# Kernel tuning notes

Measured on AMD Instinct MI355X. Metric: run time of the kernel, lower is better.

The kernel has to match this reference:

```python
import jax, jax.numpy as jnp
import numpy as np


def setup_inputs() -> dict:
    key = jax.random.key(0)
    k1, k2 = jax.random.split(key)
    n_nodes, d_feat, n_edges = 100000, 48, 1600000
    x = jax.random.normal(k1, (n_nodes, d_feat), dtype=jnp.float32)
    edge_index = jax.random.randint(k2, (2, n_edges), 0, n_nodes, dtype=jnp.int64)
    return {"x": x, "edge_index": edge_index, "batch_size": 65536}


def reference(x, edge_index, batch_size):
    # adj = SparseTensor.from_edge_index(edge_index): adj[row, col] = 1 with
    # row = edge_index[0] (src), col = edge_index[1] (dst).
    # adj.t() @ x  ->  out[i] = sum over edges (src -> i) of x[src]
    src, dst = edge_index[0], edge_index[1]
    n_nodes = x.shape[0]
    # memory-bound gather + scatter-add (SpMM, sum aggregation)
    x_neighbors_sum = jax.ops.segment_sum(x[src], dst, num_segments=n_nodes)
    node_labels = jnp.concatenate(
        (x[:batch_size, :], x_neighbors_sum[:batch_size, :]), axis=-1
    )
    return node_labels
```

## Files before the change

kernel.cpp:

```cpp
#include <hip/hip_runtime.h>

#define DFEAT 48
#define OUTW  96
#define NBINB 256
#define BINTH 512
#define SORTCAP 6272
#define NBUCK2 512
#define RBITS 7
#define NROWS 128
#define RAWCAP 2560
#define HCAP 1536


__global__ __launch_bounds__(BINTH)
void bin_k(const int* __restrict__ ei, int n_edges, int batch, int chunk,
           unsigned short* __restrict__ starts, unsigned int* __restrict__ regions) {
    __shared__ int cnt[NBUCK2];
    __shared__ int off[NBUCK2];
    __shared__ int cur[NBUCK2];
    __shared__ unsigned int sorted[SORTCAP];
    const int t = threadIdx.x;
    const int b = blockIdx.x;
    const int beg = b * chunk;
    const int end = min(beg + chunk, n_edges);

    cnt[t] = 0;
    __syncthreads();
    for (int e = beg + t; e < end; e += BINTH) {
        int dst = ei[n_edges + e];
        if (dst < batch) atomicAdd(&cnt[dst >> RBITS], 1);
    }
    __syncthreads();
    int v = cnt[t];
    off[t] = v;
    __syncthreads();
    for (int d = 1; d < NBUCK2; d <<= 1) {
        int tv = (t >= d) ? off[t - d] : 0;
        __syncthreads();
        off[t] += tv;
        __syncthreads();
    }
    int excl = off[t] - v;
    int tot  = off[NBUCK2 - 1];
    __syncthreads();
    off[t] = excl;
    cur[t] = excl;
    starts[t * NBINB + b] = (unsigned short)excl;
    if (t == 0) starts[NBUCK2 * NBINB + b] = (unsigned short)tot;
    __syncthreads();
    for (int e = beg + t; e < end; e += BINTH) {
        int dst = ei[n_edges + e];
        if (dst < batch) {
            int src = ei[e];
            int pos = atomicAdd(&cur[dst >> RBITS], 1);
            sorted[pos] = ((unsigned int)(dst & (NROWS - 1)) << 17) | (unsigned int)src;
        }
    }
    __syncthreads();
    unsigned int* reg = regions + (size_t)b * chunk;
    for (int i = t; i < tot; i += BINTH) reg[i] = sorted[i];
}

__global__ __launch_bounds__(512)
void reduce_k(const float* __restrict__ x,
              const unsigned short* __restrict__ starts,
              const unsigned int* __restrict__ regions,
              float* __restrict__ out, int batch, int chunk) {
    __shared__ unsigned int raw[RAWCAP];
    __shared__ int csr[HCAP];
    __shared__ int rs[NBINB], rp[NBINB], rl[NBINB];
    __shared__ int cnt[64], off[65], cur[64];
    __shared__ int Tsh;
    const int t = threadIdx.x;
    const int kb = blockIdx.x >> 1;
    const int half = blockIdx.x & 1;

    if (t < NBINB) {
        int s0 = starts[kb * NBINB + t];
        int s1 = starts[(kb + 1) * NBINB + t];
        rs[t] = s0;
        rl[t] = s1 - s0;
        rp[t] = s1 - s0;
    }
    __syncthreads();
    for (int d = 1; d < NBINB; d <<= 1) {
        int tv = (t < NBINB && t >= d) ? rp[t - d] : 0;
        __syncthreads();
        if (t < NBINB) rp[t] += tv;
        __syncthreads();
    }
    if (t == NBINB - 1) Tsh = rp[t];
    __syncthreads();
    const int T = min(Tsh, RAWCAP);
    if (t < NBINB) rp[t] -= rl[t];
    __syncthreads();
    {
        int r = t >> 1, h = t & 1;
        int len = rl[r], base = rp[r];
        const unsigned int* reg = regions + (size_t)r * chunk + rs[r];
        for (int i = h; i < len; i += 2) {
            int p = base + i;
            if (p < RAWCAP) raw[p] = reg[i];
        }
    }
    __syncthreads();
    if (t < 64) cnt[t] = 0;
    __syncthreads();
    for (int i = t; i < T; i += 512) {
        int rw = raw[i] >> 17;
        if ((rw >> 6) == half) atomicAdd(&cnt[rw & 63], 1);
    }
    __syncthreads();
    int v = (t < 64) ? cnt[t] : 0;
    if (t < 64) off[t] = v;
    __syncthreads();
    for (int d = 1; d < 64; d <<= 1) {
        int tv = (t < 64 && t >= d) ? off[t - d] : 0;
        __syncthreads();
        if (t < 64) off[t] += tv;
        __syncthreads();
    }
    if (t == 63) off[64] = off[63];
    int excl = (t < 64) ? off[t] - v : 0;
    __syncthreads();
    if (t < 64) { off[t] = excl; cur[t] = excl; }
    __syncthreads();
    for (int i = t; i < T; i += 512) {
        unsigned int p = raw[i];
        int rw = p >> 17;
        if ((rw >> 6) == half) {
            int pos = atomicAdd(&cur[rw & 63], 1);
            if (pos < HCAP) csr[pos] = (int)(p & 0x1FFFFu);
        }
    }
    __syncthreads();
    const int wave = t >> 6, lane = t & 63;
    if (lane < DFEAT) {
        for (int r = wave; r < 64; r += 8) {
            int row = kb * NROWS + half * 64 + r;
            if (row >= batch) break;
            int s0 = off[r], s1 = min(off[r + 1], HCAP);
            float acc = 0.f;
            int e = s0;
            for (; e + 4 <= s1; e += 4) {
                float v0 = x[(size_t)csr[e + 0] * DFEAT + lane];
                float v1 = x[(size_t)csr[e + 1] * DFEAT + lane];
                float v2 = x[(size_t)csr[e + 2] * DFEAT + lane];
                float v3 = x[(size_t)csr[e + 3] * DFEAT + lane];
                acc += v0 + v1 + v2 + v3;
            }
            for (; e < s1; ++e) acc += x[(size_t)csr[e] * DFEAT + lane];
            out[(size_t)row * OUTW + lane]         = x[(size_t)row * DFEAT + lane];
            out[(size_t)row * OUTW + DFEAT + lane] = acc;
        }
    }
}


#define D4   12
#define ROW4 24

__global__ void init_out_kernel(const float4* __restrict__ x4,
                                float4* __restrict__ out4, int batch) {
    int idx = blockIdx.x * blockDim.x + threadIdx.x;
    int total = batch * ROW4;
    if (idx >= total) return;
    int row = idx / ROW4;
    int c   = idx - row * ROW4;
    float4 v;
    if (c < D4) v = x4[row * D4 + c];
    else        v = make_float4(0.f, 0.f, 0.f, 0.f);
    out4[idx] = v;
}

__global__ void scatter_edges_kernel(const float4* __restrict__ x4,
                                     const int* __restrict__ ei,
                                     float* __restrict__ out,
                                     int n_edges, int batch) {
    int tid = blockIdx.x * blockDim.x + threadIdx.x;
    int e = tid / D4;
    int q = tid - e * D4;
    if (e >= n_edges) return;
    int dst = ei[n_edges + e];
    if (dst >= batch) return;
    int src = ei[e];
    float4 v = x4[src * D4 + q];
    float* p = out + (size_t)dst * OUTW + DFEAT + q * 4;
    atomicAdd(p + 0, v.x);
    atomicAdd(p + 1, v.y);
    atomicAdd(p + 2, v.z);
    atomicAdd(p + 3, v.w);
}


extern "C" void kernel_launch(void* const* d_in, const int* in_sizes, int n_in,
                              void* d_out, int out_size, void* d_ws, size_t ws_size,
                              hipStream_t stream) {
    const float* x  = (const float*)d_in[0];
    const int*   ei = (const int*)d_in[1];
    float* out = (float*)d_out;

    const int n_edges = in_sizes[1] / 2;
    const int batch   = out_size / OUTW;
    const int n_nodes = in_sizes[0] / DFEAT;
    const int chunk   = (n_edges + NBINB - 1) / NBINB;
    const int nbuck   = (batch + NROWS - 1) / NROWS;

    size_t starts_bytes = (size_t)(NBUCK2 + 1) * NBINB * sizeof(unsigned short);
    size_t need = starts_bytes + (size_t)NBINB * chunk * sizeof(unsigned int);

    bool ok = ws_size >= need && chunk <= SORTCAP && n_nodes <= (1 << 17) &&
              batch <= NBUCK2 * NROWS && nbuck >= 1;

    if (ok) {
        unsigned short* starts = (unsigned short*)d_ws;
        unsigned int* regions = (unsigned int*)((char*)d_ws + starts_bytes);
        bin_k<<<NBINB, BINTH, 0, stream>>>(ei, n_edges, batch, chunk, starts, regions);
        reduce_k<<<nbuck * 2, 512, 0, stream>>>(x, starts, regions, out, batch, chunk);
    } else {
        {
            int total = batch * ROW4;
            int grid = (total + 255) / 256;
            init_out_kernel<<<grid, 256, 0, stream>>>((const float4*)x,
                                                      (float4*)out, batch);
        }
        {
            long long total = (long long)n_edges * D4;
            long long grid = (total + 255) / 256;
            scatter_edges_kernel<<<(int)grid, 256, 0, stream>>>(
                (const float4*)x, ei, out, n_edges, batch);
        }
    }
}
```

Measured before the change: 135.6 us.

## Gather neighbors from fp16 copy of x, double binning blocks, register-cache edges

The binning kernel now also converts x to fp16 in workspace, and the reduce kernel gathers neighbour rows from that half-precision copy while still accumulating in fp32. The number of binning blocks doubles to 512 and each thread keeps its edges in registers, so edge_index is read once instead of twice. The reduce kernel's per-bin copy is reassigned to one thread per bin. This halves gather bytes but adds a full pass over x for conversion and introduces fp16 rounding error in the neighbour sums.

```diff
diff --git a/kernel.cpp b/kernel.cpp
--- a/kernel.cpp
+++ b/kernel.cpp
@@ -1,10 +1,12 @@
 #include <hip/hip_runtime.h>
+#include <hip/hip_fp16.h>
 
 #define DFEAT 48
 #define OUTW  96
-#define NBINB 256
+#define NBINB 512
 #define BINTH 512
-#define SORTCAP 6272
+#define EPT   7
+#define SORTCAP 3328
 #define NBUCK2 512
 #define RBITS 7
 #define NROWS 128
@@ -12,93 +14,119 @@
 #define HCAP 1536
 
 
+static __device__ __forceinline__ unsigned short f2h(float f) {
+    __half h = __float2half_rn(f);
+    return *reinterpret_cast<unsigned short*>(&h);
+}
+static __device__ __forceinline__ float h2f(unsigned short u) {
+    __half_raw hr; hr.x = u;
+    return __half2float(*reinterpret_cast<__half*>(&hr));
+}
+
 __global__ __launch_bounds__(BINTH)
 void bin_k(const int* __restrict__ ei, int n_edges, int batch, int chunk,
-           unsigned short* __restrict__ starts, unsigned int* __restrict__ regions) {
+           const float4* __restrict__ x4, int nx4, uint2* __restrict__ xh4,
+           unsigned short* __restrict__ starts, unsigned int* __restrict__ regions,
+           int use_half) {
     __shared__ int cnt[NBUCK2];
-    __shared__ int off[NBUCK2];
     __shared__ int cur[NBUCK2];
     __shared__ unsigned int sorted[SORTCAP];
     const int t = threadIdx.x;
     const int b = blockIdx.x;
+
+    if (use_half) {
+        for (int i = b * BINTH + t; i < nx4; i += NBINB * BINTH) {
+            float4 v = x4[i];
+            unsigned short h0 = f2h(v.x), h1 = f2h(v.y);
+            unsigned short h2 = f2h(v.z), h3 = f2h(v.w);
+            xh4[i] = make_uint2((unsigned)h0 | ((unsigned)h1 << 16),
+                                (unsigned)h2 | ((unsigned)h3 << 16));
+        }
+    }
+
     const int beg = b * chunk;
     const int end = min(beg + chunk, n_edges);
 
+    unsigned int pay[EPT];
+    int bkt[EPT];
+    #pragma unroll
+    for (int i = 0; i < EPT; i++) {
+        bkt[i] = -1;
+        int e = beg + t + i * BINTH;
+        if (e < end) {
+            int dst = ei[n_edges + e];
+            if (dst < batch) {
+                int src = ei[e];
+                bkt[i] = dst >> RBITS;
+                pay[i] = ((unsigned)(dst & (NROWS - 1)) << 17) | (unsigned)src;
+            }
+        }
+    }
     cnt[t] = 0;
     __syncthreads();
-    for (int e = beg + t; e < end; e += BINTH) {
-        int dst = ei[n_edges + e];
-        if (dst < batch) atomicAdd(&cnt[dst >> RBITS], 1);
-    }
+    #pragma unroll
+    for (int i = 0; i < EPT; i++)
+        if (bkt[i] >= 0) atomicAdd(&cnt[bkt[i]], 1);
     __syncthreads();
     int v = cnt[t];
-    off[t] = v;
+    cur[t] = v;
     __syncthreads();
     for (int d = 1; d < NBUCK2; d <<= 1) {
-        int tv = (t >= d) ? off[t - d] : 0;
-        __syncthreads();
-        off[t] += tv;
-        __syncthreads();
-    }
-    int excl = off[t] - v;
-    int tot  = off[NBUCK2 - 1];
-    __syncthreads();
-    off[t] = excl;
+        int tv = (t >= d) ? cur[t - d] : 0;
+        __syncthreads();
+        cur[t] += tv;
+        __syncthreads();
+    }
+    int tot  = cur[NBUCK2 - 1];
+    int excl = cur[t] - v;
+    __syncthreads();
     cur[t] = excl;
     starts[t * NBINB + b] = (unsigned short)excl;
     if (t == 0) starts[NBUCK2 * NBINB + b] = (unsigned short)tot;
     __syncthreads();
-    for (int e = beg + t; e < end; e += BINTH) {
-        int dst = ei[n_edges + e];
-        if (dst < batch) {
-            int src = ei[e];
-            int pos = atomicAdd(&cur[dst >> RBITS], 1);
-            sorted[pos] = ((unsigned int)(dst & (NROWS - 1)) << 17) | (unsigned int)src;
-        }
-    }
+    #pragma unroll
+    for (int i = 0; i < EPT; i++)
+        if (bkt[i] >= 0) {
+            int pos = atomicAdd(&cur[bkt[i]], 1);
+            sorted[pos] = pay[i];
+        }
     __syncthreads();
     unsigned int* reg = regions + (size_t)b * chunk;
     for (int i = t; i < tot; i += BINTH) reg[i] = sorted[i];
 }
 
 __global__ __launch_bounds__(512)
-void reduce_k(const float* __restrict__ x,
+void reduce_k(const float* __restrict__ x, const unsigned short* __restrict__ xh,
               const unsigned short* __restrict__ starts,
               const unsigned int* __restrict__ regions,
-              float* __restrict__ out, int batch, int chunk) {
+              float* __restrict__ out, int batch, int chunk, int use_half) {
     __shared__ unsigned int raw[RAWCAP];
     __shared__ int csr[HCAP];
     __shared__ int rs[NBINB], rp[NBINB], rl[NBINB];
     __shared__ int cnt[64], off[65], cur[64];
-    __shared__ int Tsh;
     const int t = threadIdx.x;
     const int kb = blockIdx.x >> 1;
     const int half = blockIdx.x & 1;
 
-    if (t < NBINB) {
+    {
         int s0 = starts[kb * NBINB + t];
         int s1 = starts[(kb + 1) * NBINB + t];
-        rs[t] = s0;
-        rl[t] = s1 - s0;
-        rp[t] = s1 - s0;
+        rs[t] = s0; rl[t] = s1 - s0; rp[t] = s1 - s0;
     }
     __syncthreads();
     for (int d = 1; d < NBINB; d <<= 1) {
-        int tv = (t < NBINB && t >= d) ? rp[t - d] : 0;
-        __syncthreads();
-        if (t < NBINB) rp[t] += tv;
-        __syncthreads();
-    }
-    if (t == NBINB - 1) Tsh = rp[t];
-    __syncthreads();
-    const int T = min(Tsh, RAWCAP);
-    if (t < NBINB) rp[t] -= rl[t];
+        int tv = (t >= d) ? rp[t - d] : 0;
+        __syncthreads();
+        rp[t] += tv;
+        __syncthreads();
+    }
+    const int T = min(rp[NBINB - 1], RAWCAP);
+    const int base = rp[t] - rl[t];
     __syncthreads();
     {
-        int r = t >> 1, h = t & 1;
-        int len = rl[r], base = rp[r];
-        const unsigned int* reg = regions + (size_t)r * chunk + rs[r];
-        for (int i = h; i < len; i += 2) {
+        int len = rl[t];
+        const unsigned int* reg = regions + (size_t)t * chunk + rs[t];
+        for (int i = 0; i < len; i++) {
             int p = base + i;
             if (p < RAWCAP) raw[p] = reg[i];
         }
@@ -142,14 +170,27 @@
             int s0 = off[r], s1 = min(off[r + 1], HCAP);
             float acc = 0.f;
             int e = s0;
-            for (; e + 4 <= s1; e += 4) {
-                float v0 = x[(size_t)csr[e + 0] * DFEAT + lane];
-                float v1 = x[(size_t)csr[e + 1] * DFEAT + lane];
-                float v2 = x[(size_t)csr[e + 2] * DFEAT + lane];
-                float v3 = x[(size_t)csr[e + 3] * DFEAT + lane];
-                acc += v0 + v1 + v2 + v3;
+            if (use_half) {
+                for (; e + 4 <= s1; e += 4) {
+                    float v0 = h2f(xh[(size_t)csr[e + 0] * DFEAT + lane]);
+                    float v1 = h2f(xh[(size_t)csr[e + 1] * DFEAT + lane]);
+                    float v2 = h2f(xh[(size_t)csr[e + 2] * DFEAT + lane]);
+                    float v3 = h2f(xh[(size_t)csr[e + 3] * DFEAT + lane]);
+                    acc += v0 + v1 + v2 + v3;
+                }
+                for (; e < s1; ++e)
+                    acc += h2f(xh[(size_t)csr[e] * DFEAT + lane]);
+            } else {
+                for (; e + 4 <= s1; e += 4) {
+                    float v0 = x[(size_t)csr[e + 0] * DFEAT + lane];
+                    float v1 = x[(size_t)csr[e + 1] * DFEAT + lane];
+                    float v2 = x[(size_t)csr[e + 2] * DFEAT + lane];
+                    float v3 = x[(size_t)csr[e + 3] * DFEAT + lane];
+                    acc += v0 + v1 + v2 + v3;
+                }
+                for (; e < s1; ++e)
+                    acc += x[(size_t)csr[e] * DFEAT + lane];
             }
-            for (; e < s1; ++e) acc += x[(size_t)csr[e] * DFEAT + lane];
             out[(size_t)row * OUTW + lane]         = x[(size_t)row * DFEAT + lane];
             out[(size_t)row * OUTW + DFEAT + lane] = acc;
         }
@@ -205,18 +246,36 @@
     const int n_nodes = in_sizes[0] / DFEAT;
     const int chunk   = (n_edges + NBINB - 1) / NBINB;
     const int nbuck   = (batch + NROWS - 1) / NROWS;
-
+    const int nx4     = n_nodes * DFEAT / 4;
+
+    size_t xh_bytes = ((size_t)n_nodes * DFEAT * sizeof(unsigned short) + 15) & ~(size_t)15;
     size_t starts_bytes = (size_t)(NBUCK2 + 1) * NBINB * sizeof(unsigned short);
-    size_t need = starts_bytes + (size_t)NBINB * chunk * sizeof(unsigned int);
-
-    bool ok = ws_size >= need && chunk <= SORTCAP && n_nodes <= (1 << 17) &&
-              batch <= NBUCK2 * NROWS && nbuck >= 1;
-
-    if (ok) {
+    size_t reg_bytes = (size_t)NBINB * chunk * sizeof(unsigned int);
+    size_t need_h = xh_bytes + starts_bytes + reg_bytes;
+    size_t need_f = starts_bytes + reg_bytes;
+
+    bool base_ok = chunk <= SORTCAP && chunk <= BINTH * EPT &&
+                   n_nodes <= (1 << 17) && batch <= NBUCK2 * NROWS &&
+                   (n_nodes * DFEAT) % 4 == 0 && nbuck >= 1;
+
+    if (base_ok && ws_size >= need_h) {
+        unsigned short* xh = (unsigned short*)d_ws;
+        unsigned short* starts = (unsigned short*)((char*)d_ws + xh_bytes);
+        unsigned int* regions = (unsigned int*)((char*)d_ws + xh_bytes + starts_bytes);
+        bin_k<<<NBINB, BINTH, 0, stream>>>(ei, n_edges, batch, chunk,
+                                           (const float4*)x, nx4, (uint2*)xh,
+                                           starts, regions, 1);
+        reduce_k<<<nbuck * 2, 512, 0, stream>>>(x, xh, starts, regions, out,
+                                                batch, chunk, 1);
+    } else if (base_ok && ws_size >= need_f) {
         unsigned short* starts = (unsigned short*)d_ws;
         unsigned int* regions = (unsigned int*)((char*)d_ws + starts_bytes);
-        bin_k<<<NBINB, BINTH, 0, stream>>>(ei, n_edges, batch, chunk, starts, regions);
-        reduce_k<<<nbuck * 2, 512, 0, stream>>>(x, starts, regions, out, batch, chunk);
+        bin_k<<<NBINB, BINTH, 0, stream>>>(ei, n_edges, batch, chunk,
+                                           (const float4*)x, nx4, (uint2*)0,
+                                           starts, regions, 0);
+        reduce_k<<<nbuck * 2, 512, 0, stream>>>(x, (const unsigned short*)0,
+                                                starts, regions, out,
+                                                batch, chunk, 0);
     } else {
         {
             int total = batch * ROW4;
```

New measurement: 127.3 us. 1.07x faster.
